# Performance work log

Measured on AMD Instinct MI355X. Metric: run time of the kernel, lower is better.

Reference implementation:

```python
import jax, jax.numpy as jnp
import numpy as np

EMBED = 1024
HEADS = 16
HEAD_DIM = EMBED // HEADS          # 64
EXP_DIM = 2 * HEAD_DIM             # 128


def setup_inputs() -> dict:
    key = jax.random.key(0)
    ks = jax.random.split(key, 7)
    N, S = 4, 2048
    values = jax.random.normal(ks[0], (N, S, EMBED), dtype=jnp.float32)
    keys_ = jax.random.normal(ks[1], (N, S, EMBED), dtype=jnp.float32)
    query = jax.random.normal(ks[2], (N, S, EMBED), dtype=jnp.float32)
    # feature map linear: initialized to identity weight, zero bias (per init_weights),
    # perturb slightly so it's a nontrivial learned map
    fm_w = jnp.eye(HEAD_DIM, dtype=jnp.float32) + 0.02 * jax.random.normal(ks[3], (HEAD_DIM, HEAD_DIM), dtype=jnp.float32)
    fm_b = 0.02 * jax.random.normal(ks[4], (HEAD_DIM,), dtype=jnp.float32)
    fc_w = jax.random.normal(ks[5], (EMBED, HEADS * EXP_DIM), dtype=jnp.float32) * (1.0 / np.sqrt(HEADS * EXP_DIM))
    fc_b = jnp.zeros((EMBED,), dtype=jnp.float32)
    return {"values": values, "keys": keys_, "query": query,
            "fm_w": fm_w, "fm_b": fm_b, "fc_w": fc_w, "fc_b": fc_b}


def _feature_map(x, fm_w, fm_b):
    # x: [n, s, h, d] -> [n, s, h, 2d]
    z = jnp.einsum('nshd,ed->nshe', x, fm_w) + fm_b
    return jnp.concatenate([jnp.exp(z), jnp.exp(-z)], axis=-1)


def reference(values, keys, query, fm_w, fm_b, fc_w, fc_b):
    N, S, _ = query.shape
    v = values.reshape(N, -1, HEADS, HEAD_DIM)
    k = keys.reshape(N, -1, HEADS, HEAD_DIM)
    q = query.reshape(N, -1, HEADS, HEAD_DIM)
    v, k, q = (_feature_map(x, fm_w, fm_b) for x in (v, k, q))  # [n,s,h,2d]
    scores = jnp.einsum('nqhd,nkhd->nhqk', q, k) / jnp.sqrt(jnp.float32(EMBED))
    attn = jax.nn.softmax(scores, axis=-1)
    out = jnp.einsum('nhql,nlhd->nqhd', attn, v)  # [n,q,h,2d]
    out = out.reshape(N, S, HEADS * EXP_DIM)
    return out @ fc_w.T + fc_b
```

## Files before the change

kernel.cpp:

```cpp
#include <hip/hip_runtime.h>
#include <hip/hip_bf16.h>
#include <stdint.h>

#define N_B 4
#define SEQ 2048
#define NH 16
#define ED 128
#define EMB 1024
#define FCK 2048

typedef float f32x4 __attribute__((ext_vector_type(4)));
typedef float f32x16 __attribute__((ext_vector_type(16)));
typedef _Float16 f16x8 __attribute__((ext_vector_type(8)));
typedef _Float16 f16x4 __attribute__((ext_vector_type(4)));
typedef _Float16 f16x2 __attribute__((ext_vector_type(2)));
typedef __fp16 fp16v2 __attribute__((ext_vector_type(2)));

__device__ __forceinline__ void gload16(const void* g, void* l) {
    __builtin_amdgcn_global_load_lds(
        (const __attribute__((address_space(1))) uint32_t*)(g),
        (__attribute__((address_space(3))) uint32_t*)(l), 16, 0, 0);
}

__device__ __forceinline__ int pk2(float a, float b) {
    union { fp16v2 h; int i; } u;
    u.h = __builtin_amdgcn_cvt_pkrtz(a, b);
    return u.i;
}

__device__ __forceinline__ f16x2 asf16x2(int v) {
    union { int i; f16x2 h; } u; u.i = v; return u.h;
}

__device__ __forceinline__ f16x8 frag4(int d0, int d1, int d2, int d3) {
    union { int i[4]; f16x8 v; } u;
    u.i[0] = d0; u.i[1] = d1; u.i[2] = d2; u.i[3] = d3;
    return u.v;
}

__device__ __forceinline__ float ex2(float x) {
#if __has_builtin(__builtin_amdgcn_exp2f)
    return __builtin_amdgcn_exp2f(x);
#else
    return exp2f(x);
#endif
}

#define M3(a,b,c) fmaxf(fmaxf((a),(b)),(c))

__global__ __launch_bounds__(256) void fmap_kernel(
    const float* __restrict__ vals, const float* __restrict__ keys,
    const float* __restrict__ qry,  const float* __restrict__ fmw,
    const float* __restrict__ fmb,
    _Float16* __restrict__ qf, _Float16* __restrict__ kf,
    _Float16* __restrict__ vf)
{
    const int lane = threadIdx.x & 63;
    const int w = threadIdx.x >> 6;
    const int t = blockIdx.x * 4 + w;
    const int n = t >> 11;
    const int s = t & 2047;
    const int r = lane & 15;
    const int g = lane >> 4;

    f16x8 whf[4][2], wlf[4][2];
    #pragma unroll
    for (int te = 0; te < 4; ++te) {
      #pragma unroll
      for (int j = 0; j < 2; ++j) {
        const float* p = fmw + (te*16 + r)*64 + j*32 + 8*g;
        #pragma unroll
        for (int i = 0; i < 8; ++i) {
            float wv = p[i];
            _Float16 hi = (_Float16)wv;
            whf[te][j][i] = hi;
            wlf[te][j][i] = (_Float16)(wv - (float)hi);
        }
      }
    }
    float bias[4];
    #pragma unroll
    for (int te = 0; te < 4; ++te) bias[te] = fmb[te*16 + r];

    const float QSCL = 0.03125f * 1.4426950408889634f;

    const long rowoff = ((long)t*16 + r) * 64;
    const float* srcs[3] = {qry, keys, vals};
    #pragma unroll
    for (int tens = 0; tens < 3; ++tens) {
        const float* src = srcs[tens] + rowoff;
        f16x8 ah[2], al[2];
        #pragma unroll
        for (int j = 0; j < 2; ++j) {
            #pragma unroll
            for (int i = 0; i < 8; ++i) {
                float x = src[j*32 + 8*g + i];
                _Float16 hi = (_Float16)x;
                ah[j][i] = hi;
                al[j][i] = (_Float16)(x - (float)hi);
            }
        }
        #pragma unroll
        for (int te = 0; te < 4; ++te) {
            f32x4 c = (f32x4){0.f,0.f,0.f,0.f};
            c = __builtin_amdgcn_mfma_f32_16x16x32_f16(ah[0], whf[te][0], c, 0, 0, 0);
            c = __builtin_amdgcn_mfma_f32_16x16x32_f16(ah[1], whf[te][1], c, 0, 0, 0);
            c = __builtin_amdgcn_mfma_f32_16x16x32_f16(ah[0], wlf[te][0], c, 0, 0, 0);
            c = __builtin_amdgcn_mfma_f32_16x16x32_f16(ah[1], wlf[te][1], c, 0, 0, 0);
            c = __builtin_amdgcn_mfma_f32_16x16x32_f16(al[0], whf[te][0], c, 0, 0, 0);
            c = __builtin_amdgcn_mfma_f32_16x16x32_f16(al[1], whf[te][1], c, 0, 0, 0);
            #pragma unroll
            for (int i = 0; i < 4; ++i) {
                float z = c[i] + bias[te];
                float ep = __expf(z), en = __expf(-z);
                int hh = 4*g + i;
                int e = te*16 + r;
                long base = (((long)n*NH + hh)*SEQ + s)*ED;
                if (tens == 0) {
                    qf[base + e]      = (_Float16)(ep * QSCL);
                    qf[base + 64 + e] = (_Float16)(en * QSCL);
                } else if (tens == 1) {
                    kf[base + e]      = (_Float16)ep;
                    kf[base + 64 + e] = (_Float16)en;
                } else {
                    vf[base + e]      = (_Float16)ep;
                    vf[base + 64 + e] = (_Float16)en;
                }
            }
        }
    }
}

__global__ __launch_bounds__(256) void vtrans_kernel(
    const _Float16* __restrict__ vf, _Float16* __restrict__ vt)
{
    __shared__ _Float16 tile[64][72];
    const int b = blockIdx.x;
    const int et = b & 1;
    const int st = (b >> 1) & 31;
    const int nh = b >> 6;
    const _Float16* src = vf + ((long)nh*SEQ + st*64)*ED + et*64;
    const int col4 = (threadIdx.x & 15) * 4;
    const int row0 = threadIdx.x >> 4;
    #pragma unroll
    for (int j = 0; j < 4; ++j) {
        int row = row0 + j*16;
        *(f16x4*)&tile[row][col4] = *(const f16x4*)(src + (long)row*ED + col4);
    }
    __syncthreads();
    _Float16* dst = vt + ((long)nh*ED + et*64)*SEQ + st*64;
    const int erow = threadIdx.x >> 2;
    const int sc0 = (threadIdx.x & 3) * 16;
    f16x8 o0, o1;
    #pragma unroll
    for (int i = 0; i < 8; ++i) o0[i] = tile[sc0 + i][erow];
    #pragma unroll
    for (int i = 0; i < 8; ++i) o1[i] = tile[sc0 + 8 + i][erow];
    *(f16x8*)(dst + (long)erow*SEQ + sc0) = o0;
    *(f16x8*)(dst + (long)erow*SEQ + sc0 + 8) = o1;
}

__global__ __launch_bounds__(256) void cvt_kernel(
    const float* __restrict__ src, _Float16* __restrict__ dst)
{
    long i = ((long)blockIdx.x*256 + threadIdx.x)*8;
    f16x8 o;
    #pragma unroll
    for (int j = 0; j < 8; ++j) o[j] = (_Float16)src[i + j];
    *(f16x8*)(dst + i) = o;
}

__global__ __launch_bounds__(512, 2) void attn_kernel(
    const _Float16* __restrict__ qf,
    const _Float16* __restrict__ kf,
    const _Float16* __restrict__ vt,
    _Float16* __restrict__ ob)
{
    __shared__ char smem[131072];
    const int tid = threadIdx.x;
    const int lane = tid & 63;
    const int w = tid >> 6;
    const int orig = blockIdx.x;
    const int b = ((orig & 7) << 6) | (orig >> 3);
    const int nh = b >> 3;
    const int n = nh >> 4, h = nh & 15;
    const int qt = (b & 7)*8 + w;
    const int q32 = lane & 31;
    const int hl = lane >> 5;

    const _Float16* qb = qf + (long)nh*SEQ*ED;
    const char* kg = (const char*)(kf + (long)nh*SEQ*ED);
    const char* vg = (const char*)(vt + (long)nh*ED*SEQ);

    f16x8 qfr[8];
    #pragma unroll
    for (int j = 0; j < 8; ++j)
        qfr[j] = *(const f16x8*)(qb + (long)(qt*32 + q32)*ED + 16*j + 8*hl);

    const int srow = tid >> 4;
    const int sc   = (tid & 15) ^ (srow & 15);
    const long koff = (long)srow*256  + sc*16;
    const long voff = (long)srow*4096 + sc*16;
    const int  ldst = tid*16;

    auto stage = [&](int kt, int bsel) {
        char* Kl = smem + bsel*65536;
        char* Vl = Kl + 32768;
        const char* ksrc = kg + (long)kt*32768 + koff;
        const char* vsrc = vg + (long)kt*256   + voff;
        #pragma unroll
        for (int i = 0; i < 4; ++i)
            gload16(ksrc + i*8192, Kl + i*8192 + ldst);
        #pragma unroll
        for (int i = 0; i < 4; ++i)
            gload16(vsrc + (long)i*131072, Vl + i*8192 + ldst);
    };

    f32x16 acc[4];
    #pragma unroll
    for (int vv = 0; vv < 4; ++vv)
      #pragma unroll
      for (int i = 0; i < 16; ++i) acc[vv][i] = 0.f;
    float mrun = 0.f, lrun = 0.f;

    stage(0, 0);
    __syncthreads();

    const int kswz = q32 & 15;

    for (int kt = 0; kt < SEQ/128; ++kt) {
        const int cur = kt & 1;
        if (kt + 1 < SEQ/128) stage(kt + 1, cur ^ 1);
        const char* Kl = smem + cur*65536;
        const char* Vl = Kl + 32768;

        #pragma unroll
        for (int p = 0; p < 2; ++p) {
            const float nmr = -mrun;
            f32x16 s0, s1;
            #pragma unroll
            for (int i = 0; i < 16; ++i) { s0[i] = nmr; s1[i] = nmr; }
            const char* Kb = Kl + (p*64 + q32)*256;
            __builtin_amdgcn_s_setprio(1);
            #pragma unroll
            for (int j = 0; j < 8; ++j) {
                int off = (((hl + 2*j) & 15) ^ kswz) << 4;
                f16x8 k0 = *(const f16x8*)(Kb + off);
                f16x8 k1 = *(const f16x8*)(Kb + 8192 + off);
                s0 = __builtin_amdgcn_mfma_f32_32x32x16_f16(k0, qfr[j], s0, 0, 0, 0);
                s1 = __builtin_amdgcn_mfma_f32_32x32x16_f16(k1, qfr[j], s1, 0, 0, 0);
            }
            __builtin_amdgcn_s_setprio(0);

            float mx = M3(s0[0], s0[1], s0[2]);
            mx = M3(mx, s0[3], s0[4]);   mx = M3(mx, s0[5], s0[6]);
            mx = M3(mx, s0[7], s0[8]);   mx = M3(mx, s0[9], s0[10]);
            mx = M3(mx, s0[11], s0[12]); mx = M3(mx, s0[13], s0[14]);
            mx = M3(mx, s0[15], s1[0]);  mx = M3(mx, s1[1], s1[2]);
            mx = M3(mx, s1[3], s1[4]);   mx = M3(mx, s1[5], s1[6]);
            mx = M3(mx, s1[7], s1[8]);   mx = M3(mx, s1[9], s1[10]);
            mx = M3(mx, s1[11], s1[12]); mx = M3(mx, s1[13], s1[14]);
            mx = fmaxf(mx, s1[15]);
            mx = fmaxf(mx, __shfl_xor(mx, 32, 64));
            if (__any(mx > 8.0f)) {
                float d = fmaxf(mx, 0.f);
                float corr = ex2(-d);
                mrun += d;
                lrun *= corr;
                #pragma unroll
                for (int vv = 0; vv < 4; ++vv)
                    #pragma unroll
                    for (int i = 0; i < 16; ++i) acc[vv][i] *= corr;
                #pragma unroll
                for (int i = 0; i < 16; ++i) { s0[i] -= d; s1[i] -= d; }
            }
            int wreg[2][8];
            f16x2 psum = (f16x2){(_Float16)0.f, (_Float16)0.f};
            #pragma unroll
            for (int kk = 0; kk < 2; ++kk) {
                #pragma unroll
                for (int tW = 0; tW < 8; ++tW) {
                    float sa = (kk == 0) ? s0[2*tW]   : s1[2*tW];
                    float sb = (kk == 0) ? s0[2*tW+1] : s1[2*tW+1];
                    int pw = pk2(ex2(sa), ex2(sb));
                    wreg[kk][tW] = pw;
                    psum += asf16x2(pw);
                }
            }
            float rsum = (float)psum[0] + (float)psum[1];
            rsum += __shfl_xor(rsum, 32, 64);
            lrun += rsum;

            f16x8 pa[4];
            #pragma unroll
            for (int kk = 0; kk < 2; ++kk) {
                #pragma unroll
                for (int par = 0; par < 2; ++par) {
                    int a0 = wreg[kk][par*4 + 0], b0 = wreg[kk][par*4 + 2];
                    int a1 = wreg[kk][par*4 + 1], b1 = wreg[kk][par*4 + 3];
                    auto r0 = __builtin_amdgcn_permlane32_swap(a0, b0, false, false);
                    auto r1 = __builtin_amdgcn_permlane32_swap(a1, b1, false, false);
                    pa[kk*2 + par] = frag4(r0[0], r1[0], r0[1], r1[1]);
                }
            }

            #pragma unroll
            for (int ks = 0; ks < 4; ++ks) {
                f16x8 vfr[4];
                #pragma unroll
                for (int vv = 0; vv < 4; ++vv) {
                    int vrow = vv*32 + q32;
                    int c0 = p*8 + ks*2 + hl;
                    vfr[vv] = *(const f16x8*)(Vl + vrow*256 + ((c0 ^ kswz) << 4));
                }
                __builtin_amdgcn_s_setprio(1);
                #pragma unroll
                for (int vv = 0; vv < 4; ++vv)
                    acc[vv] = __builtin_amdgcn_mfma_f32_32x32x16_f16(vfr[vv], pa[ks], acc[vv], 0, 0, 0);
                __builtin_amdgcn_s_setprio(0);
            }
        }
        __syncthreads();
    }

    float inv = 1.0f / lrun;
    int q = qt*32 + q32;
    long base = ((long)n*SEQ + q)*FCK + h*ED;
    #pragma unroll
    for (int vv = 0; vv < 4; ++vv) {
        #pragma unroll
        for (int rg = 0; rg < 4; ++rg) {
            f16x4 o;
            #pragma unroll
            for (int i = 0; i < 4; ++i) o[i] = (_Float16)(acc[vv][rg*4 + i] * inv);
            *(f16x4*)(ob + base + vv*32 + 8*rg + 4*hl) = o;
        }
    }
}

__global__ __launch_bounds__(256) void fc_kernel(
    const _Float16* __restrict__ ob,
    const _Float16* __restrict__ wt,
    const float* __restrict__ fcb,
    float* __restrict__ out)
{
    __shared__ char smem[32768];
    const int lane = threadIdx.x & 63;
    const int w = threadIdx.x >> 6;
    const int wm = w >> 1, wn = w & 1;
    const int r = lane & 15, g = lane >> 4;

    const int orig = blockIdx.x;
    const int tile = ((orig & 7) << 6) | (orig >> 3);
    const int mt = tile >> 3;
    const int nt = tile & 7;

    const char* Ag = (const char*)(ob + (long)mt*128*FCK);
    const char* Bg = (const char*)(wt + (long)nt*128*FCK);

    auto stage = [&](int kt, int bsel) {
        char* As = smem + bsel*16384;
        char* Bs = As + 8192;
        #pragma unroll
        for (int rnd = 0; rnd < 2; ++rnd) {
            int row = rnd*64 + w*16 + (lane >> 2);
            int cs = (lane & 3) ^ ((row >> 1) & 3);
            gload16(Ag + (long)row*(FCK*2) + kt*64 + cs*16, As + rnd*4096 + w*1024);
            gload16(Bg + (long)row*(FCK*2) + kt*64 + cs*16, Bs + rnd*4096 + w*1024);
        }
    };

    f32x4 acc[4][4];
    #pragma unroll
    for (int u = 0; u < 4; ++u)
      #pragma unroll
      for (int v = 0; v < 4; ++v) acc[u][v] = (f32x4){0.f,0.f,0.f,0.f};

    stage(0, 0);
    __syncthreads();

    for (int kt = 0; kt < FCK/32; ++kt) {
        const int cur = kt & 1;
        if (kt + 1 < FCK/32) stage(kt + 1, cur ^ 1);
        const char* As = smem + cur*16384;
        const char* Bs = As + 8192;

        f16x8 afr[4], bfr[4];
        #pragma unroll
        for (int u = 0; u < 4; ++u) {
            int row = wm*64 + u*16 + r;
            afr[u] = *(const f16x8*)(As + row*64 + ((g ^ ((row >> 1) & 3)) << 4));
        }
        #pragma unroll
        for (int v = 0; v < 4; ++v) {
            int row = wn*64 + v*16 + r;
            bfr[v] = *(const f16x8*)(Bs + row*64 + ((g ^ ((row >> 1) & 3)) << 4));
        }
        __builtin_amdgcn_s_setprio(1);
        #pragma unroll
        for (int u = 0; u < 4; ++u)
          #pragma unroll
          for (int v = 0; v < 4; ++v)
            acc[u][v] = __builtin_amdgcn_mfma_f32_16x16x32_f16(afr[u], bfr[v], acc[u][v], 0, 0, 0);
        __builtin_amdgcn_s_setprio(0);
        __syncthreads();
    }

    #pragma unroll
    for (int u = 0; u < 4; ++u)
      #pragma unroll
      for (int v = 0; v < 4; ++v) {
        int col = nt*128 + wn*64 + v*16 + r;
        float bias = fcb[col];
        #pragma unroll
        for (int i = 0; i < 4; ++i) {
            int row = mt*128 + wm*64 + u*16 + 4*g + i;
            out[(long)row*EMB + col] = acc[u][v][i] + bias;
        }
      }
}

extern "C" void kernel_launch(void* const* d_in, const int* in_sizes, int n_in,
                              void* d_out, int out_size, void* d_ws, size_t ws_size,
                              hipStream_t stream) {
    const float* vals = (const float*)d_in[0];
    const float* keys = (const float*)d_in[1];
    const float* qry  = (const float*)d_in[2];
    const float* fmw  = (const float*)d_in[3];
    const float* fmb  = (const float*)d_in[4];
    const float* fcw  = (const float*)d_in[5];
    const float* fcb  = (const float*)d_in[6];
    char* ws = (char*)d_ws;
    const long SZ = 33554432L;
    _Float16* qf = (_Float16*)(ws);
    _Float16* kf = (_Float16*)(ws + SZ);
    _Float16* vf = (_Float16*)(ws + 2*SZ);
    _Float16* vt = (_Float16*)(ws + 3*SZ);
    _Float16* ob = (_Float16*)(ws + 4*SZ);
    _Float16* wt = (_Float16*)(ws + 5*SZ);
    float* out = (float*)d_out;

    fmap_kernel<<<dim3(2048), dim3(256), 0, stream>>>(vals, keys, qry, fmw, fmb, qf, kf, vf);
    vtrans_kernel<<<dim3(4096), dim3(256), 0, stream>>>(vf, vt);
    cvt_kernel<<<dim3(1024), dim3(256), 0, stream>>>(fcw, wt);
    attn_kernel<<<dim3(512), dim3(512), 0, stream>>>(qf, kf, vt, ob);
    fc_kernel<<<dim3(512), dim3(256), 0, stream>>>(ob, wt, fcb, out);
}
```

Before: 269.9 us.

## Software-pipeline QK^T of second half-tile ahead of softmax of first half

Unrolls the two 64-key halves of each K/V tile by hand and issues both QK^T MFMA chains before doing softmax on the first half. The second half's score MFMAs can then overlap with the first half's exp, pack and PV work, hiding softmax VALU latency behind matrix ops. The cost is another 32 live accumulator registers, which may raise VGPR pressure or cause spills. The setprio placement also changes.

```diff
diff --git a/kernel.cpp b/kernel.cpp
--- a/kernel.cpp
+++ b/kernel.cpp
@@ -234,92 +234,168 @@
         const char* Kl = smem + cur*65536;
         const char* Vl = Kl + 32768;
 
-        #pragma unroll
-        for (int p = 0; p < 2; ++p) {
-            const float nmr = -mrun;
-            f32x16 s0, s1;
-            #pragma unroll
-            for (int i = 0; i < 16; ++i) { s0[i] = nmr; s1[i] = nmr; }
-            const char* Kb = Kl + (p*64 + q32)*256;
-            __builtin_amdgcn_s_setprio(1);
-            #pragma unroll
-            for (int j = 0; j < 8; ++j) {
-                int off = (((hl + 2*j) & 15) ^ kswz) << 4;
-                f16x8 k0 = *(const f16x8*)(Kb + off);
-                f16x8 k1 = *(const f16x8*)(Kb + 8192 + off);
-                s0 = __builtin_amdgcn_mfma_f32_32x32x16_f16(k0, qfr[j], s0, 0, 0, 0);
-                s1 = __builtin_amdgcn_mfma_f32_32x32x16_f16(k1, qfr[j], s1, 0, 0, 0);
-            }
-            __builtin_amdgcn_s_setprio(0);
-
-            float mx = M3(s0[0], s0[1], s0[2]);
-            mx = M3(mx, s0[3], s0[4]);   mx = M3(mx, s0[5], s0[6]);
-            mx = M3(mx, s0[7], s0[8]);   mx = M3(mx, s0[9], s0[10]);
-            mx = M3(mx, s0[11], s0[12]); mx = M3(mx, s0[13], s0[14]);
-            mx = M3(mx, s0[15], s1[0]);  mx = M3(mx, s1[1], s1[2]);
-            mx = M3(mx, s1[3], s1[4]);   mx = M3(mx, s1[5], s1[6]);
-            mx = M3(mx, s1[7], s1[8]);   mx = M3(mx, s1[9], s1[10]);
-            mx = M3(mx, s1[11], s1[12]); mx = M3(mx, s1[13], s1[14]);
-            mx = fmaxf(mx, s1[15]);
-            mx = fmaxf(mx, __shfl_xor(mx, 32, 64));
-            if (__any(mx > 8.0f)) {
-                float d = fmaxf(mx, 0.f);
-                float corr = ex2(-d);
-                mrun += d;
-                lrun *= corr;
+        const float nmr = -mrun;
+        f32x16 sA0, sA1;
+        #pragma unroll
+        for (int i = 0; i < 16; ++i) { sA0[i] = nmr; sA1[i] = nmr; }
+        const char* KbA = Kl + q32*256;
+        __builtin_amdgcn_s_setprio(1);
+        #pragma unroll
+        for (int j = 0; j < 8; ++j) {
+            int off = (((hl + 2*j) & 15) ^ kswz) << 4;
+            f16x8 k0 = *(const f16x8*)(KbA + off);
+            f16x8 k1 = *(const f16x8*)(KbA + 8192 + off);
+            sA0 = __builtin_amdgcn_mfma_f32_32x32x16_f16(k0, qfr[j], sA0, 0, 0, 0);
+            sA1 = __builtin_amdgcn_mfma_f32_32x32x16_f16(k1, qfr[j], sA1, 0, 0, 0);
+        }
+        __builtin_amdgcn_s_setprio(0);
+
+        f32x16 sB0, sB1;
+        #pragma unroll
+        for (int i = 0; i < 16; ++i) { sB0[i] = nmr; sB1[i] = nmr; }
+        const char* KbB = Kl + (64 + q32)*256;
+        #pragma unroll
+        for (int j = 0; j < 8; ++j) {
+            int off = (((hl + 2*j) & 15) ^ kswz) << 4;
+            f16x8 k0 = *(const f16x8*)(KbB + off);
+            f16x8 k1 = *(const f16x8*)(KbB + 8192 + off);
+            sB0 = __builtin_amdgcn_mfma_f32_32x32x16_f16(k0, qfr[j], sB0, 0, 0, 0);
+            sB1 = __builtin_amdgcn_mfma_f32_32x32x16_f16(k1, qfr[j], sB1, 0, 0, 0);
+        }
+
+        float mxA = M3(sA0[0], sA0[1], sA0[2]);
+        mxA = M3(mxA, sA0[3], sA0[4]);   mxA = M3(mxA, sA0[5], sA0[6]);
+        mxA = M3(mxA, sA0[7], sA0[8]);   mxA = M3(mxA, sA0[9], sA0[10]);
+        mxA = M3(mxA, sA0[11], sA0[12]); mxA = M3(mxA, sA0[13], sA0[14]);
+        mxA = M3(mxA, sA0[15], sA1[0]);  mxA = M3(mxA, sA1[1], sA1[2]);
+        mxA = M3(mxA, sA1[3], sA1[4]);   mxA = M3(mxA, sA1[5], sA1[6]);
+        mxA = M3(mxA, sA1[7], sA1[8]);   mxA = M3(mxA, sA1[9], sA1[10]);
+        mxA = M3(mxA, sA1[11], sA1[12]); mxA = M3(mxA, sA1[13], sA1[14]);
+        mxA = fmaxf(mxA, sA1[15]);
+        mxA = fmaxf(mxA, __shfl_xor(mxA, 32, 64));
+        if (__any(mxA > 8.0f)) {
+            float d = fmaxf(mxA, 0.f);
+            float corr = ex2(-d);
+            mrun += d;
+            lrun *= corr;
+            #pragma unroll
+            for (int vv = 0; vv < 4; ++vv)
                 #pragma unroll
-                for (int vv = 0; vv < 4; ++vv)
-                    #pragma unroll
-                    for (int i = 0; i < 16; ++i) acc[vv][i] *= corr;
+                for (int i = 0; i < 16; ++i) acc[vv][i] *= corr;
+            #pragma unroll
+            for (int i = 0; i < 16; ++i) {
+                sA0[i] -= d; sA1[i] -= d;
+                sB0[i] -= d; sB1[i] -= d;
+            }
+        }
+        int wregA[2][8];
+        f16x2 psumA = (f16x2){(_Float16)0.f, (_Float16)0.f};
+        #pragma unroll
+        for (int tW = 0; tW < 8; ++tW) {
+            int pw = pk2(ex2(sA0[2*tW]), ex2(sA0[2*tW+1]));
+            wregA[0][tW] = pw; psumA += asf16x2(pw);
+        }
+        #pragma unroll
+        for (int tW = 0; tW < 8; ++tW) {
+            int pw = pk2(ex2(sA1[2*tW]), ex2(sA1[2*tW+1]));
+            wregA[1][tW] = pw; psumA += asf16x2(pw);
+        }
+        float rsumA = (float)psumA[0] + (float)psumA[1];
+        rsumA += __shfl_xor(rsumA, 32, 64);
+        lrun += rsumA;
+        f16x8 paA[4];
+        #pragma unroll
+        for (int kk = 0; kk < 2; ++kk) {
+            #pragma unroll
+            for (int par = 0; par < 2; ++par) {
+                int a0 = wregA[kk][par*4 + 0], b0 = wregA[kk][par*4 + 2];
+                int a1 = wregA[kk][par*4 + 1], b1 = wregA[kk][par*4 + 3];
+                auto r0 = __builtin_amdgcn_permlane32_swap(a0, b0, false, false);
+                auto r1 = __builtin_amdgcn_permlane32_swap(a1, b1, false, false);
+                paA[kk*2 + par] = frag4(r0[0], r1[0], r0[1], r1[1]);
+            }
+        }
+
+        #pragma unroll
+        for (int ks = 0; ks < 4; ++ks) {
+            f16x8 vfr[4];
+            #pragma unroll
+            for (int vv = 0; vv < 4; ++vv) {
+                int vrow = vv*32 + q32;
+                int c0 = ks*2 + hl;
+                vfr[vv] = *(const f16x8*)(Vl + vrow*256 + ((c0 ^ kswz) << 4));
+            }
+            #pragma unroll
+            for (int vv = 0; vv < 4; ++vv)
+                acc[vv] = __builtin_amdgcn_mfma_f32_32x32x16_f16(vfr[vv], paA[ks], acc[vv], 0, 0, 0);
+        }
+
+        float mxB = M3(sB0[0], sB0[1], sB0[2]);
+        mxB = M3(mxB, sB0[3], sB0[4]);   mxB = M3(mxB, sB0[5], sB0[6]);
+        mxB = M3(mxB, sB0[7], sB0[8]);   mxB = M3(mxB, sB0[9], sB0[10]);
+        mxB = M3(mxB, sB0[11], sB0[12]); mxB = M3(mxB, sB0[13], sB0[14]);
+        mxB = M3(mxB, sB0[15], sB1[0]);  mxB = M3(mxB, sB1[1], sB1[2]);
+        mxB = M3(mxB, sB1[3], sB1[4]);   mxB = M3(mxB, sB1[5], sB1[6]);
+        mxB = M3(mxB, sB1[7], sB1[8]);   mxB = M3(mxB, sB1[9], sB1[10]);
+        mxB = M3(mxB, sB1[11], sB1[12]); mxB = M3(mxB, sB1[13], sB1[14]);
+        mxB = fmaxf(mxB, sB1[15]);
+        mxB = fmaxf(mxB, __shfl_xor(mxB, 32, 64));
+        if (__any(mxB > 8.0f)) {
+            float d = fmaxf(mxB, 0.f);
+            float corr = ex2(-d);
+            mrun += d;
+            lrun *= corr;
+            #pragma unroll
+            for (int vv = 0; vv < 4; ++vv)
                 #pragma unroll
-                for (int i = 0; i < 16; ++i) { s0[i] -= d; s1[i] -= d; }
-            }
-            int wreg[2][8];
-            f16x2 psum = (f16x2){(_Float16)0.f, (_Float16)0.f};
-            #pragma unroll
-            for (int kk = 0; kk < 2; ++kk) {
-                #pragma unroll
-                for (int tW = 0; tW < 8; ++tW) {
-                    float sa = (kk == 0) ? s0[2*tW]   : s1[2*tW];
-                    float sb = (kk == 0) ? s0[2*tW+1] : s1[2*tW+1];
-                    int pw = pk2(ex2(sa), ex2(sb));
-                    wreg[kk][tW] = pw;
-                    psum += asf16x2(pw);
-                }
-            }
-            float rsum = (float)psum[0] + (float)psum[1];
-            rsum += __shfl_xor(rsum, 32, 64);
-            lrun += rsum;
-
-            f16x8 pa[4];
-            #pragma unroll
-            for (int kk = 0; kk < 2; ++kk) {
-                #pragma unroll
-                for (int par = 0; par < 2; ++par) {
-                    int a0 = wreg[kk][par*4 + 0], b0 = wreg[kk][par*4 + 2];
-                    int a1 = wreg[kk][par*4 + 1], b1 = wreg[kk][par*4 + 3];
-                    auto r0 = __builtin_amdgcn_permlane32_swap(a0, b0, false, false);
-                    auto r1 = __builtin_amdgcn_permlane32_swap(a1, b1, false, false);
-                    pa[kk*2 + par] = frag4(r0[0], r1[0], r0[1], r1[1]);
-                }
-            }
-
-            #pragma unroll
-            for (int ks = 0; ks < 4; ++ks) {
-                f16x8 vfr[4];
-                #pragma unroll
-                for (int vv = 0; vv < 4; ++vv) {
-                    int vrow = vv*32 + q32;
-                    int c0 = p*8 + ks*2 + hl;
-                    vfr[vv] = *(const f16x8*)(Vl + vrow*256 + ((c0 ^ kswz) << 4));
-                }
-                __builtin_amdgcn_s_setprio(1);
-                #pragma unroll
-                for (int vv = 0; vv < 4; ++vv)
-                    acc[vv] = __builtin_amdgcn_mfma_f32_32x32x16_f16(vfr[vv], pa[ks], acc[vv], 0, 0, 0);
-                __builtin_amdgcn_s_setprio(0);
-            }
-        }
+                for (int i = 0; i < 16; ++i) acc[vv][i] *= corr;
+            #pragma unroll
+            for (int i = 0; i < 16; ++i) { sB0[i] -= d; sB1[i] -= d; }
+        }
+        int wregB[2][8];
+        f16x2 psumB = (f16x2){(_Float16)0.f, (_Float16)0.f};
+        #pragma unroll
+        for (int tW = 0; tW < 8; ++tW) {
+            int pw = pk2(ex2(sB0[2*tW]), ex2(sB0[2*tW+1]));
+            wregB[0][tW] = pw; psumB += asf16x2(pw);
+        }
+        #pragma unroll
+        for (int tW = 0; tW < 8; ++tW) {
+            int pw = pk2(ex2(sB1[2*tW]), ex2(sB1[2*tW+1]));
+            wregB[1][tW] = pw; psumB += asf16x2(pw);
+        }
+        float rsumB = (float)psumB[0] + (float)psumB[1];
+        rsumB += __shfl_xor(rsumB, 32, 64);
+        lrun += rsumB;
+        f16x8 paB[4];
+        #pragma unroll
+        for (int kk = 0; kk < 2; ++kk) {
+            #pragma unroll
+            for (int par = 0; par < 2; ++par) {
+                int a0 = wregB[kk][par*4 + 0], b0 = wregB[kk][par*4 + 2];
+                int a1 = wregB[kk][par*4 + 1], b1 = wregB[kk][par*4 + 3];
+                auto r0 = __builtin_amdgcn_permlane32_swap(a0, b0, false, false);
+                auto r1 = __builtin_amdgcn_permlane32_swap(a1, b1, false, false);
+                paB[kk*2 + par] = frag4(r0[0], r1[0], r0[1], r1[1]);
+            }
+        }
+
+        __builtin_amdgcn_s_setprio(1);
+        #pragma unroll
+        for (int ks = 0; ks < 4; ++ks) {
+            f16x8 vfr[4];
+            #pragma unroll
+            for (int vv = 0; vv < 4; ++vv) {
+                int vrow = vv*32 + q32;
+                int c0 = 8 + ks*2 + hl;
+                vfr[vv] = *(const f16x8*)(Vl + vrow*256 + ((c0 ^ kswz) << 4));
+            }
+            #pragma unroll
+            for (int vv = 0; vv < 4; ++vv)
+                acc[vv] = __builtin_amdgcn_mfma_f32_32x32x16_f16(vfr[vv], paB[ks], acc[vv], 0, 0, 0);
+        }
+        __builtin_amdgcn_s_setprio(0);
+
         __syncthreads();
     }
 
```

New measurement: 270.1 us. Within noise of the previous version (+0.1%).

## Double fc kernel K-tile to 64 with 8-chunk swizzle; use exp2 in feature map

Applied to the files above, without the earlier changes.

The fc GEMM kernel now stages 64-wide K tiles (128 bytes per row) into 64KB of double-buffered LDS. It uses a new 8-chunk XOR swizzle and per-thread contiguous global-to-LDS loads, which halves the number of barriers and pipeline iterations. The feature-map kernel replaces __expf with a scaled hardware exp2, and the attention softmax exp loop is split into two plain loops. The larger LDS footprint may reduce fc kernel occupancy.

```diff
diff --git a/kernel.cpp b/kernel.cpp
--- a/kernel.cpp
+++ b/kernel.cpp
@@ -46,6 +46,7 @@
 #endif
 }
 
+#define LOG2E 1.4426950408889634f
 #define M3(a,b,c) fmaxf(fmaxf((a),(b)),(c))
 
 __global__ __launch_bounds__(256) void fmap_kernel(
@@ -82,7 +83,7 @@
     #pragma unroll
     for (int te = 0; te < 4; ++te) bias[te] = fmb[te*16 + r];
 
-    const float QSCL = 0.03125f * 1.4426950408889634f;
+    const float QSCL = 0.03125f * LOG2E;
 
     const long rowoff = ((long)t*16 + r) * 64;
     const float* srcs[3] = {qry, keys, vals};
@@ -111,8 +112,8 @@
             c = __builtin_amdgcn_mfma_f32_16x16x32_f16(al[1], whf[te][1], c, 0, 0, 0);
             #pragma unroll
             for (int i = 0; i < 4; ++i) {
-                float z = c[i] + bias[te];
-                float ep = __expf(z), en = __expf(-z);
+                float zl = (c[i] + bias[te]) * LOG2E;
+                float ep = ex2(zl), en = ex2(-zl);
                 int hh = 4*g + i;
                 int e = te*16 + r;
                 long base = (((long)n*NH + hh)*SEQ + s)*ED;
@@ -277,15 +278,14 @@
             int wreg[2][8];
             f16x2 psum = (f16x2){(_Float16)0.f, (_Float16)0.f};
             #pragma unroll
-            for (int kk = 0; kk < 2; ++kk) {
-                #pragma unroll
-                for (int tW = 0; tW < 8; ++tW) {
-                    float sa = (kk == 0) ? s0[2*tW]   : s1[2*tW];
-                    float sb = (kk == 0) ? s0[2*tW+1] : s1[2*tW+1];
-                    int pw = pk2(ex2(sa), ex2(sb));
-                    wreg[kk][tW] = pw;
-                    psum += asf16x2(pw);
-                }
+            for (int tW = 0; tW < 8; ++tW) {
+                int pw = pk2(ex2(s0[2*tW]), ex2(s0[2*tW+1]));
+                wreg[0][tW] = pw; psum += asf16x2(pw);
+            }
+            #pragma unroll
+            for (int tW = 0; tW < 8; ++tW) {
+                int pw = pk2(ex2(s1[2*tW]), ex2(s1[2*tW+1]));
+                wreg[1][tW] = pw; psum += asf16x2(pw);
             }
             float rsum = (float)psum[0] + (float)psum[1];
             rsum += __shfl_xor(rsum, 32, 64);
@@ -344,9 +344,10 @@
     const float* __restrict__ fcb,
     float* __restrict__ out)
 {
-    __shared__ char smem[32768];
-    const int lane = threadIdx.x & 63;
-    const int w = threadIdx.x >> 6;
+    __shared__ char smem[65536];
+    const int tid = threadIdx.x;
+    const int lane = tid & 63;
+    const int w = tid >> 6;
     const int wm = w >> 1, wn = w & 1;
     const int r = lane & 15, g = lane >> 4;
 
@@ -358,16 +359,22 @@
     const char* Ag = (const char*)(ob + (long)mt*128*FCK);
     const char* Bg = (const char*)(wt + (long)nt*128*FCK);
 
+    const int srow = tid >> 3;
+    const int schk = tid & 7;
+    const int  ldst = tid*16;
+    const long goff = (long)srow*(FCK*2) + (schk ^ (srow & 7))*16;
+
     auto stage = [&](int kt, int bsel) {
-        char* As = smem + bsel*16384;
-        char* Bs = As + 8192;
-        #pragma unroll
-        for (int rnd = 0; rnd < 2; ++rnd) {
-            int row = rnd*64 + w*16 + (lane >> 2);
-            int cs = (lane & 3) ^ ((row >> 1) & 3);
-            gload16(Ag + (long)row*(FCK*2) + kt*64 + cs*16, As + rnd*4096 + w*1024);
-            gload16(Bg + (long)row*(FCK*2) + kt*64 + cs*16, Bs + rnd*4096 + w*1024);
-        }
+        char* As = smem + bsel*32768;
+        char* Bs = As + 16384;
+        const char* asrc = Ag + (long)kt*128 + goff;
+        const char* bsrc = Bg + (long)kt*128 + goff;
+        #pragma unroll
+        for (int rnd = 0; rnd < 4; ++rnd)
+            gload16(asrc + (long)rnd*32*(FCK*2), As + rnd*4096 + ldst);
+        #pragma unroll
+        for (int rnd = 0; rnd < 4; ++rnd)
+            gload16(bsrc + (long)rnd*32*(FCK*2), Bs + rnd*4096 + ldst);
     };
 
     f32x4 acc[4][4];
@@ -379,30 +386,33 @@
     stage(0, 0);
     __syncthreads();
 
-    for (int kt = 0; kt < FCK/32; ++kt) {
+    for (int kt = 0; kt < FCK/64; ++kt) {
         const int cur = kt & 1;
-        if (kt + 1 < FCK/32) stage(kt + 1, cur ^ 1);
-        const char* As = smem + cur*16384;
-        const char* Bs = As + 8192;
-
-        f16x8 afr[4], bfr[4];
-        #pragma unroll
-        for (int u = 0; u < 4; ++u) {
-            int row = wm*64 + u*16 + r;
-            afr[u] = *(const f16x8*)(As + row*64 + ((g ^ ((row >> 1) & 3)) << 4));
-        }
-        #pragma unroll
-        for (int v = 0; v < 4; ++v) {
-            int row = wn*64 + v*16 + r;
-            bfr[v] = *(const f16x8*)(Bs + row*64 + ((g ^ ((row >> 1) & 3)) << 4));
-        }
-        __builtin_amdgcn_s_setprio(1);
-        #pragma unroll
-        for (int u = 0; u < 4; ++u)
-          #pragma unroll
-          for (int v = 0; v < 4; ++v)
-            acc[u][v] = __builtin_amdgcn_mfma_f32_16x16x32_f16(afr[u], bfr[v], acc[u][v], 0, 0, 0);
-        __builtin_amdgcn_s_setprio(0);
+        if (kt + 1 < FCK/64) stage(kt + 1, cur ^ 1);
+        const char* As = smem + cur*32768;
+        const char* Bs = As + 16384;
+
+        #pragma unroll
+        for (int kk = 0; kk < 2; ++kk) {
+            f16x8 afr[4], bfr[4];
+            #pragma unroll
+            for (int u = 0; u < 4; ++u) {
+                int row = wm*64 + u*16 + r;
+                afr[u] = *(const f16x8*)(As + row*128 + (((g + 4*kk) ^ (row & 7)) << 4));
+            }
+            #pragma unroll
+            for (int v = 0; v < 4; ++v) {
+                int row = wn*64 + v*16 + r;
+                bfr[v] = *(const f16x8*)(Bs + row*128 + (((g + 4*kk) ^ (row & 7)) << 4));
+            }
+            __builtin_amdgcn_s_setprio(1);
+            #pragma unroll
+            for (int u = 0; u < 4; ++u)
+              #pragma unroll
+              for (int v = 0; v < 4; ++v)
+                acc[u][v] = __builtin_amdgcn_mfma_f32_16x16x32_f16(afr[u], bfr[v], acc[u][v], 0, 0, 0);
+            __builtin_amdgcn_s_setprio(0);
+        }
         __syncthreads();
     }
 
```

Result: no change. 266.3 us (-1.3%).
